# Kernel tuning notes

Hardware: AMD Instinct MI355X
Metric: run time of the kernel (lower is better)

## Reference

```python
import jax, jax.numpy as jnp
import numpy as np

IH, IW = 256, 704
FH, FW = 32, 88
D_MIN, D_MAX, D_RES = 1.0, 60.0, 0.5
D = int(np.ceil((D_MAX - D_MIN) / D_RES))  # 118 depth bins
C_IN, HID, C_OUT = 256, 64, 80
N_R, N_THETA = 128, 256
BN_EPS = 1e-5


def _edges():
    # non-uniform polar grid: angular bins uniform, radial bins grow with r
    ang = np.linspace(-np.pi / 2, np.pi / 2, N_THETA + 1).astype(np.float32)
    t = np.linspace(0.0, 1.0, N_R + 1)
    rad = (D_MIN + (t ** 1.5) * (D_MAX - D_MIN)).astype(np.float32)
    return jnp.asarray(ang), jnp.asarray(rad)


def _frustum():
    # [D, fH, fW, 3] of (u, v, depth) samples in image space
    ds = np.arange(D_MIN, D_MAX, D_RES, dtype=np.float32)
    xs = np.linspace(0, IW - 1, FW, dtype=np.float32)
    ys = np.linspace(0, IH - 1, FH, dtype=np.float32)
    d = np.broadcast_to(ds[:, None, None], (D, FH, FW))
    x = np.broadcast_to(xs[None, None, :], (D, FH, FW))
    y = np.broadcast_to(ys[None, :, None], (D, FH, FW))
    return jnp.asarray(np.stack([x, y, d], axis=-1))


def _bn(x, g, b, m, v):
    # inference-mode BatchNorm2d over channel axis 1; x: [BN, C, H, W]
    inv = g / jnp.sqrt(v + BN_EPS)
    return x * inv[None, :, None, None] + (b - m * inv)[None, :, None, None]


def setup_inputs() -> dict:
    key = jax.random.key(0)
    ks = jax.random.split(key, 8)
    B, N = 2, 1
    x = jax.random.normal(ks[0], (B, N, C_IN, FH, FW), dtype=jnp.float32)
    # camera->lidar axis permutation: x_l = z_c, y_l = -x_c, z_l = -y_c
    R = jnp.asarray([[0.0, 0.0, 1.0], [-1.0, 0.0, 0.0], [0.0, -1.0, 0.0]], dtype=jnp.float32)
    camera2lidar_rots = jnp.broadcast_to(R, (B, N, 3, 3))
    camera2lidar_trans = jnp.zeros((B, N, 3), dtype=jnp.float32)
    K = jnp.asarray([[380.0, 0.0, IW / 2.0], [0.0, 380.0, IH / 2.0], [0.0, 0.0, 1.0]], dtype=jnp.float32)
    intrins = jnp.broadcast_to(K, (B, N, 3, 3))
    s = 0.02
    params = dict(
        w1=jax.random.normal(ks[1], (HID, C_IN), dtype=jnp.float32) * s,
        b1=jnp.zeros((HID,), dtype=jnp.float32),
        g1=jnp.ones((HID,), dtype=jnp.float32),
        be1=jnp.zeros((HID,), dtype=jnp.float32),
        m1=jax.random.normal(ks[2], (HID,), dtype=jnp.float32) * s,
        v1=jnp.abs(jax.random.normal(ks[3], (HID,), dtype=jnp.float32)) + 0.5,
        w2=jax.random.normal(ks[4], (D + C_OUT, HID), dtype=jnp.float32) * s,
        b2=jnp.zeros((D + C_OUT,), dtype=jnp.float32),
        g2=jnp.ones((D + C_OUT,), dtype=jnp.float32),
        be2=jnp.zeros((D + C_OUT,), dtype=jnp.float32),
        m2=jax.random.normal(ks[5], (D + C_OUT,), dtype=jnp.float32) * s,
        v2=jnp.abs(jax.random.normal(ks[6], (D + C_OUT,), dtype=jnp.float32)) + 0.5,
    )
    return dict(x=x, camera2lidar_rots=camera2lidar_rots,
                camera2lidar_trans=camera2lidar_trans, intrins=intrins, **params)


def reference(x, camera2lidar_rots, camera2lidar_trans, intrins,
              w1, b1, g1, be1, m1, v1, w2, b2, g2, be2, m2, v2):
    B, N = x.shape[0], x.shape[1]
    # --- LIFT: DepthNet (two 1x1 convs + BN) -> depth dist x features outer product ---
    xf = x.reshape(B * N, C_IN, FH, FW)
    h = jnp.einsum('bchw,oc->bohw', xf, w1) + b1[None, :, None, None]
    h = jax.nn.relu(_bn(h, g1, be1, m1, v1))
    h = jnp.einsum('bchw,oc->bohw', h, w2) + b2[None, :, None, None]
    h = _bn(h, g2, be2, m2, v2)
    depth = jax.nn.softmax(h[:, :D], axis=1)            # [BN, D, fH, fW]
    feat = h[:, D:D + C_OUT]                            # [BN, C, fH, fW]
    lifted = depth[:, None, :, :, :] * feat[:, :, None, :, :]   # [BN, C, D, fH, fW]
    lifted = lifted.reshape(B, N, C_OUT, D, FH, FW).transpose(0, 1, 3, 4, 5, 2)  # [B,N,D,fH,fW,C]

    # --- geometry: unproject frustum to lidar frame ---
    fr = _frustum()                                      # [D, fH, fW, 3]
    u, v_, d = fr[..., 0], fr[..., 1], fr[..., 2]
    fx = intrins[..., 0, 0][:, :, None, None, None]
    fy = intrins[..., 1, 1][:, :, None, None, None]
    cx = intrins[..., 0, 2][:, :, None, None, None]
    cy = intrins[..., 1, 2][:, :, None, None, None]
    pc = jnp.stack([(u - cx) * d / fx, (v_ - cy) * d / fy,
                    jnp.broadcast_to(d, (B, N, D, FH, FW))], axis=-1)  # [B,N,D,fH,fW,3]
    pts = jnp.einsum('bnij,bndhwj->bndhwi', camera2lidar_rots, pc)
    pts = pts + camera2lidar_trans[:, :, None, None, None, :]

    # --- SPLAT: scatter-sum into non-uniform polar BEV grid ---
    ang_e, rad_e = _edges()
    xl, yl = pts[..., 0], pts[..., 1]
    r = jnp.sqrt(xl * xl + yl * yl)
    th = jnp.arctan2(yl, xl)
    r_idx = jnp.searchsorted(rad_e, r, side='right') - 1   # non-uniform bins -> bucketize
    t_idx = jnp.searchsorted(ang_e, th, side='right') - 1
    valid = (r_idx >= 0) & (r_idx < N_R) & (t_idx >= 0) & (t_idx < N_THETA)
    b_idx = jnp.arange(B)[:, None, None, None, None]
    trash = B * N_R * N_THETA  # dummy segment for out-of-grid points
    seg = jnp.where(valid, (b_idx * N_R + r_idx) * N_THETA + t_idx, trash).reshape(-1)
    bev = jax.ops.segment_sum(lifted.reshape(-1, C_OUT), seg, num_segments=trash + 1)[:-1]
    bev = bev.reshape(B, N_R, N_THETA, C_OUT).transpose(0, 3, 1, 2)  # [B, C, n_r, n_theta]
    return bev
```

## Files before the change

kernel.cpp:

```cpp
#include <hip/hip_runtime.h>
#include <hip/hip_bf16.h>
#include <math.h>

#define FH 32
#define FW 88
#define DD 118
#define C_IN 256
#define HID 64
#define C_OUT 80
#define NPIX 5632
#define PIX_PER_B 2816
#define N_R 128
#define N_THETA 256
#define NCOL 176
#define NBIN 32768
#define ECAP 12
#define PSTRIDE 9440

typedef __attribute__((ext_vector_type(8))) short short8;
typedef __attribute__((ext_vector_type(4))) float f32x4;

__device__ inline float bf2f(unsigned short h) {
  return __uint_as_float((unsigned)h << 16);
}
__device__ inline unsigned short f2bf(float f) {
  unsigned u = __float_as_uint(f);
  unsigned r = (u + 0x7fffu + ((u >> 16) & 1u)) >> 16;
  return (unsigned short)r;
}
__device__ inline bool detect_bf16(const void* intr) {
  float f = __uint_as_float(*(const unsigned*)intr);
  return !(f > 300.0f && f < 500.0f);
}
__device__ inline float ldf(const void* p, int i, bool isb) {
  return isb ? bf2f(((const unsigned short*)p)[i]) : ((const float*)p)[i];
}

__device__ inline void load_geom(int tid, float* radEL, float* angEL, float* camsL,
                                 const void* rots, const void* trans, const void* intr,
                                 bool isb) {
  if (tid < 129) {
    double t = (double)tid * (1.0 / 128.0);
    radEL[tid] = (float)(1.0 + pow(t, 1.5) * 59.0);
  }
  for (int i = tid; i < 257; i += 256) {
    double step = M_PI / 256.0;
    double vv = (i == 256) ? (M_PI / 2.0) : ((double)i * step + (-M_PI / 2.0));
    angEL[i] = (float)vv;
  }
  if (tid < 18) camsL[tid] = ldf(rots, tid, isb);
  if (tid < 6)  camsL[20 + tid] = ldf(trans, tid, isb);
  if (tid >= 6 && tid < 24) camsL[28 + (tid - 6)] = ldf(intr, tid - 6, isb);
}

__device__ inline int computeBin(int w, int h, int d,
                                 const float* camsF, int b,
                                 const float* radE, const float* angE) {
  float fx = camsF[28 + b * 9 + 0], cx = camsF[28 + b * 9 + 2];
  float fy = camsF[28 + b * 9 + 4], cy = camsF[28 + b * 9 + 5];
  float R00 = camsF[b * 9 + 0], R01 = camsF[b * 9 + 1], R02 = camsF[b * 9 + 2];
  float R10 = camsF[b * 9 + 3], R11 = camsF[b * 9 + 4], R12 = camsF[b * 9 + 5];
  float Tx = camsF[20 + b * 3 + 0], Ty = camsF[20 + b * 3 + 1];
  float u  = (w == FW - 1) ? 703.0f : (float)((double)w * (703.0 / 87.0));
  float vv = (h == FH - 1) ? 255.0f : (float)((double)h * (255.0 / 31.0));
  float dd = 1.0f + 0.5f * (float)d;
  float px = __fdiv_rn(__fmul_rn(__fsub_rn(u, cx), dd), fx);
  float py = __fdiv_rn(__fmul_rn(__fsub_rn(vv, cy), dd), fy);
  float xl = __fadd_rn(__fadd_rn(__fadd_rn(__fmul_rn(R00, px), __fmul_rn(R01, py)),
                                 __fmul_rn(R02, dd)), Tx);
  float yl = __fadd_rn(__fadd_rn(__fadd_rn(__fmul_rn(R10, px), __fmul_rn(R11, py)),
                                 __fmul_rn(R12, dd)), Ty);
  float r = __fsqrt_rn(__fadd_rn(__fmul_rn(xl, xl), __fmul_rn(yl, yl)));
  float th = (float)atan2((double)yl, (double)xl);
  int lo = 0, hi = 129;
  while (lo < hi) { int mid = (lo + hi) >> 1; if (radE[mid] <= r) lo = mid + 1; else hi = mid; }
  int ri = lo - 1;
  lo = 0; hi = 257;
  while (lo < hi) { int mid = (lo + hi) >> 1; if (angE[mid] <= th) lo = mid + 1; else hi = mid; }
  int ti = lo - 1;
  bool valid = (ri >= 0) && (ri < N_R) && (ti >= 0) && (ti < N_THETA);
  return valid ? (ri * N_THETA + ti) : -1;
}

__global__ __launch_bounds__(256) void k_bins(const void* __restrict__ rots,
                                              const void* __restrict__ trans,
                                              const void* __restrict__ intr,
                                              const void* __restrict__ b1r, const void* __restrict__ g1r,
                                              const void* __restrict__ be1r, const void* __restrict__ m1r,
                                              const void* __restrict__ v1r,
                                              const void* __restrict__ w2r, const void* __restrict__ b2r,
                                              const void* __restrict__ g2r, const void* __restrict__ be2r,
                                              const void* __restrict__ m2r, const void* __restrict__ v2r,
                                              int* __restrict__ cnt,
                                              unsigned* __restrict__ ent,
                                              int* __restrict__ flag,
                                              float* __restrict__ w2f, float* __restrict__ b2f,
                                              float* __restrict__ inv1G, float* __restrict__ b1fG) {
  int tid = threadIdx.x;
  bool isb = detect_bf16(intr);
  if (blockIdx.x >= 2640) {
    int j = (blockIdx.x - 2640) * 256 + tid;
    if (j < 12672) {
      int o = j >> 6;
      float iv = ldf(g2r, o, isb) / sqrtf(ldf(v2r, o, isb) + 1e-5f);
      w2f[j] = ldf(w2r, j, isb) * iv;
    } else if (j < 12870) {
      int o = j - 12672;
      float iv = ldf(g2r, o, isb) / sqrtf(ldf(v2r, o, isb) + 1e-5f);
      b2f[o] = ldf(b2r, o, isb) * iv + (ldf(be2r, o, isb) - ldf(m2r, o, isb) * iv);
    } else if (j < 12934) {
      int o = j - 12870;
      float iv = ldf(g1r, o, isb) / sqrtf(ldf(v1r, o, isb) + 1e-5f);
      inv1G[o] = iv;
      b1fG[o] = ldf(b1r, o, isb) * iv + (ldf(be1r, o, isb) - ldf(m1r, o, isb) * iv);
    }
    return;
  }
  __shared__ float radEL[129], angEL[257], camsL[46];
  __shared__ int bin0[8];
  __shared__ int varMask;
  int col = blockIdx.x / 15;
  int dchunk = blockIdx.x - col * 15;
  int b = col / FW, w = col - b * FW;
  int sub = tid >> 5, h = tid & 31;
  int d = dchunk * 8 + sub;
  if (tid == 0) varMask = 0;
  load_geom(tid, radEL, angEL, camsL, rots, trans, intr, isb);
  __syncthreads();
  int bin = -1;
  if (d < DD) bin = computeBin(w, h, d, camsL, b, radEL, angEL);
  if (d < DD && h == 0) bin0[sub] = bin;
  __syncthreads();
  if (d < DD && bin != bin0[sub]) atomicOr(&varMask, 1);
  __syncthreads();
  if (h == 0 && d < DD) {
    if (varMask) atomicOr(flag, 1);
    if (bin >= 0) {
      int slot = atomicAdd(&cnt[b * NBIN + bin], 1);
      if (slot < ECAP) ent[(size_t)(b * NBIN + bin) * ECAP + slot] = ((unsigned)col << 8) | (unsigned)d;
      else atomicOr(flag, 1);
    }
  }
}

__global__ __launch_bounds__(256) void k_mlp(const void* __restrict__ xraw,
                                             const void* __restrict__ intrRaw,
                                             const void* __restrict__ w1r,
                                             const float* __restrict__ w2f,
                                             const float* __restrict__ b2f,
                                             const float* __restrict__ inv1G,
                                             const float* __restrict__ b1fG,
                                             float* __restrict__ depthW,
                                             float* __restrict__ featW) {
  __shared__ __align__(16) float shbuf[3712];
  __shared__ __align__(16) float h1L[16 * 68];
  unsigned short* xsU = (unsigned short*)shbuf;
  float* h2s = shbuf;
  float* smaxL = shbuf + 3200;
  float* ssumL = shbuf + 3456;
  int tid = threadIdx.x;
  bool isb = detect_bf16(intrRaw);
  int pix0 = blockIdx.x * 16;
  int b = pix0 / PIX_PER_B;
  int ploc0 = pix0 - b * PIX_PER_B;
  size_t xbase = (size_t)b * C_IN * PIX_PER_B + ploc0;
  const unsigned short* xh = (const unsigned short*)xraw;
  const float* xf = (const float*)xraw;
  {
    int p = tid & 15, crow = tid >> 4;
    for (int it = 0; it < 16; it++) {
      int c = it * 16 + crow;
      size_t gi = xbase + (size_t)c * PIX_PER_B + p;
      xsU[p * 264 + c] = isb ? xh[gi] : f2bf(xf[gi]);
    }
  }
  int lane = tid & 63, wv = tid >> 6;
  int nloc = lane & 15, quad = lane >> 4;
  int orow = wv * 16 + nloc;
  short8 afr[8];
  const unsigned short* w1h = (const unsigned short*)w1r;
  const float* w1f32 = (const float*)w1r;
  if (isb) {
#pragma unroll
    for (int s = 0; s < 8; s++)
      afr[s] = *(const short8*)(w1h + orow * 256 + s * 32 + quad * 8);
  } else {
#pragma unroll
    for (int s = 0; s < 8; s++) {
      short8 a;
#pragma unroll
      for (int j = 0; j < 8; j++)
        a[j] = (short)f2bf(w1f32[orow * 256 + s * 32 + quad * 8 + j]);
      afr[s] = a;
    }
  }
  __syncthreads();
  f32x4 acc = {0.f, 0.f, 0.f, 0.f};
#pragma unroll
  for (int s = 0; s < 8; s++) {
    short8 bfr = *(const short8*)(xsU + nloc * 264 + s * 32 + quad * 8);
    acc = __builtin_amdgcn_mfma_f32_16x16x32_bf16(afr[s], bfr, acc, 0, 0, 0);
  }
#pragma unroll
  for (int r = 0; r < 4; r++) {
    int m = wv * 16 + quad * 4 + r;
    float hv = fmaxf(fmaf(acc[r], inv1G[m], b1fG[m]), 0.f);
    h1L[nloc * 68 + m] = hv;
  }
  __syncthreads();
  int p = tid & 15, g = tid >> 4;
  float h1v[64];
  const float4* hp = (const float4*)(h1L + p * 68);
#pragma unroll
  for (int k4 = 0; k4 < 16; k4++) {
    float4 hv = hp[k4];
    h1v[4 * k4 + 0] = hv.x; h1v[4 * k4 + 1] = hv.y;
    h1v[4 * k4 + 2] = hv.z; h1v[4 * k4 + 3] = hv.w;
  }
  for (int j = 0; j < 13; j++) {
    int o = g * 13 + j;
    if (o < 198) {
      float accs = b2f[o];
      const float4* wr = (const float4*)(w2f + o * 64);
#pragma unroll
      for (int k4 = 0; k4 < 16; k4++) {
        float4 w = wr[k4];
        accs = fmaf(w.x, h1v[4 * k4 + 0], accs);
        accs = fmaf(w.y, h1v[4 * k4 + 1], accs);
        accs = fmaf(w.z, h1v[4 * k4 + 2], accs);
        accs = fmaf(w.w, h1v[4 * k4 + 3], accs);
      }
      h2s[o * 16 + p] = accs;
    }
  }
  __syncthreads();
  int r0 = g * 8, r1 = min(118, r0 + 8);
  float lm = -INFINITY;
  for (int o = r0; o < r1; o++) lm = fmaxf(lm, h2s[o * 16 + p]);
  smaxL[g * 16 + p] = lm;
  __syncthreads();
  float m = smaxL[p];
#pragma unroll
  for (int gg = 1; gg < 16; gg++) m = fmaxf(m, smaxL[gg * 16 + p]);
  float ls = 0.f;
  for (int o = r0; o < r1; o++) ls += expf(h2s[o * 16 + p] - m);
  ssumL[g * 16 + p] = ls;
  __syncthreads();
  float tot = 0.f;
#pragma unroll
  for (int gg = 0; gg < 16; gg++) tot += ssumL[gg * 16 + p];
  int pix = pix0 + p;
  for (int o = r0; o < r1; o++)
    depthW[(size_t)pix * DD + o] = expf(h2s[o * 16 + p] - m) / tot;
  int f0 = g * 5;
  for (int f = f0; f < f0 + 5; f++)
    featW[(size_t)pix * C_OUT + f] = h2s[(118 + f) * 16 + p];
}

__global__ __launch_bounds__(256) void k_pcol(const float* __restrict__ depthW,
                                              const float* __restrict__ featW,
                                              const int* __restrict__ flag,
                                              float* __restrict__ P,
                                              float* __restrict__ bevAcc) {
  __shared__ float depthL[DD * 33];
  __shared__ __align__(16) float featL[FH * C_OUT];
  __shared__ int flagS;
  int tid = threadIdx.x;
  int col = blockIdx.x;
  int b = col / FW, w = col - b * FW;
  if (tid == 0) flagS = *flag;
  __syncthreads();
  if (flagS != 0) {
    float4 z = make_float4(0.f, 0.f, 0.f, 0.f);
    float4* bz = (float4*)bevAcc;
    for (int i = blockIdx.x * 256 + tid; i < (NBIN * 2 * C_OUT) / 4; i += 176 * 256) bz[i] = z;
    return;
  }
  size_t colPix = (size_t)b * PIX_PER_B + w;
  for (int i = tid; i < FH * DD; i += 256) {
    int h = i / DD, d = i - h * DD;
    depthL[d * 33 + h] = depthW[(colPix + (size_t)h * FW) * DD + d];
  }
  for (int i = tid; i < FH * C_OUT; i += 256) {
    int h = i / C_OUT, c = i - h * C_OUT;
    featL[i] = featW[(colPix + (size_t)h * FW) * C_OUT + c];
  }
  __syncthreads();
  const float4* featL4 = (const float4*)featL;
  float4* P4 = (float4*)(P + (size_t)col * PSTRIDE);
  for (int t = tid; t < DD * 20; t += 256) {
    int d = t / 20, c4 = t - d * 20;
    float4 a = make_float4(0.f, 0.f, 0.f, 0.f);
#pragma unroll
    for (int h = 0; h < FH; h++) {
      float wd = depthL[d * 33 + h];
      float4 f = featL4[h * 20 + c4];
      a.x = fmaf(wd, f.x, a.x); a.y = fmaf(wd, f.y, a.y);
      a.z = fmaf(wd, f.z, a.z); a.w = fmaf(wd, f.w, a.w);
    }
    P4[d * 20 + c4] = a;
  }
}

__global__ __launch_bounds__(256) void k_fb(const float* __restrict__ depthW,
                                            const float* __restrict__ featW,
                                            const int* __restrict__ flag,
                                            const void* __restrict__ rots,
                                            const void* __restrict__ trans,
                                            const void* __restrict__ intr,
                                            float* __restrict__ bevAcc) {
  if (*flag == 0) return;
  __shared__ float radEL[129], angEL[257], camsL[46];
  __shared__ float depthL[DD * 33];
  __shared__ __align__(16) float featL[FH * C_OUT];
  int tid = threadIdx.x;
  bool isb = detect_bf16(intr);
  int col = blockIdx.x >> 1, chalf = blockIdx.x & 1;
  int b = col / FW, w = col - b * FW;
  load_geom(tid, radEL, angEL, camsL, rots, trans, intr, isb);
  size_t colPix = (size_t)b * PIX_PER_B + w;
  for (int i = tid; i < FH * DD; i += 256) {
    int h = i / DD, d = i - h * DD;
    depthL[d * 33 + h] = depthW[(colPix + (size_t)h * FW) * DD + d];
  }
  for (int i = tid; i < FH * C_OUT; i += 256) {
    int h = i / C_OUT, c = i - h * C_OUT;
    featL[i] = featW[(colPix + (size_t)h * FW) * C_OUT + c];
  }
  __syncthreads();
  const float4* featL4 = (const float4*)featL;
  for (int t = tid; t < DD * FH * 10; t += 256) {
    int d = t / 320, rem = t - d * 320;
    int h = rem / 10, c4 = chalf * 10 + (rem - (rem / 10) * 10);
    int bin = computeBin(w, h, d, camsL, b, radEL, angEL);
    if (bin < 0) continue;
    float wd = depthL[d * 33 + h];
    float4 f = featL4[h * 20 + c4];
    float* outb = bevAcc + (((size_t)(b * C_OUT + c4 * 4)) << 15) + bin;
    unsafeAtomicAdd(outb, wd * f.x);
    unsafeAtomicAdd(outb + (1u << 15), wd * f.y);
    unsafeAtomicAdd(outb + (2u << 15), wd * f.z);
    unsafeAtomicAdd(outb + (3u << 15), wd * f.w);
  }
}

__global__ __launch_bounds__(256) void k_out(const float* __restrict__ P,
                                             const int* __restrict__ cnt,
                                             const unsigned* __restrict__ ent,
                                             const int* __restrict__ flag,
                                             const float* __restrict__ bevAcc,
                                             void* __restrict__ out,
                                             const void* __restrict__ intrRaw) {
  bool isb = detect_bf16(intrRaw);
  int tid = threadIdx.x;
  if (*flag != 0) {
    int idx = blockIdx.x * 256 + tid;
    const float4* a4 = (const float4*)bevAcc;
    int n4 = (NBIN * 2 * C_OUT) / 4;
    if (isb) {
      ushort4* o4 = (ushort4*)out;
      for (int i = idx; i < n4; i += 256 * 256) {
        float4 v = a4[i];
        ushort4 o; o.x = f2bf(v.x); o.y = f2bf(v.y); o.z = f2bf(v.z); o.w = f2bf(v.w);
        o4[i] = o;
      }
    } else {
      float4* o4 = (float4*)out;
      for (int i = idx; i < n4; i += 256 * 256) o4[i] = a4[i];
    }
    return;
  }
  int b = blockIdx.x >> 7, ri = blockIdx.x & 127;
  int ti = tid;
  int bin = ri * N_THETA + ti;
  int n = cnt[b * NBIN + bin];
  if (n > ECAP) n = ECAP;
  unsigned ee[ECAP];
  const unsigned* eb = ent + (size_t)(b * NBIN + bin) * ECAP;
  for (int i = 0; i < n; i++) ee[i] = eb[i];
  for (int i = 1; i < n; i++) {
    unsigned key = ee[i]; int j = i - 1;
    while (j >= 0 && ee[j] > key) { ee[j + 1] = ee[j]; j--; }
    ee[j + 1] = key;
  }
  int base[ECAP];
  for (int i = 0; i < n; i++)
    base[i] = (int)(((ee[i] >> 8) * PSTRIDE + (ee[i] & 255u) * C_OUT) >> 2);
  const float4* P4 = (const float4*)P;
  unsigned short* oh = (unsigned short*)out;
  float* of = (float*)out;
  size_t obase = (((size_t)(b * C_OUT)) << 15) + bin;
  for (int c4 = 0; c4 < 20; c4++) {
    float4 s = make_float4(0.f, 0.f, 0.f, 0.f);
    for (int i = 0; i < n; i++) {
      float4 v = P4[base[i] + c4];
      s.x += v.x; s.y += v.y; s.z += v.z; s.w += v.w;
    }
    size_t o0 = obase + ((size_t)(c4 * 4) << 15);
    if (isb) {
      oh[o0]              = f2bf(s.x);
      oh[o0 + (1u << 15)] = f2bf(s.y);
      oh[o0 + (2u << 15)] = f2bf(s.z);
      oh[o0 + (3u << 15)] = f2bf(s.w);
    } else {
      of[o0]              = s.x;
      of[o0 + (1u << 15)] = s.y;
      of[o0 + (2u << 15)] = s.z;
      of[o0 + (3u << 15)] = s.w;
    }
  }
}

extern "C" void kernel_launch(void* const* d_in, const int* in_sizes, int n_in,
                              void* d_out, int out_size, void* d_ws, size_t ws_size,
                              hipStream_t stream) {
  const void* x     = d_in[0];
  const void* rots  = d_in[1];
  const void* trans = d_in[2];
  const void* intr  = d_in[3];
  const void* w1  = d_in[4];
  const void* b1  = d_in[5];
  const void* g1  = d_in[6];
  const void* be1 = d_in[7];
  const void* m1  = d_in[8];
  const void* v1  = d_in[9];
  const void* w2  = d_in[10];
  const void* b2  = d_in[11];
  const void* g2  = d_in[12];
  const void* be2 = d_in[13];
  const void* m2  = d_in[14];
  const void* v2  = d_in[15];

  float* ws = (float*)d_ws;
  float*    bevAcc = ws + 0;
  float*    P      = ws + 0;
  int*      cnt    = (int*)(ws + 1661440);
  int*      flag   = (int*)(ws + 1726976);
  unsigned* ent    = (unsigned*)(ws + 1727040);
  float*    depthW = ws + 5242880;
  float*    featW  = ws + 5907456;
  float*    w2f    = ws + 6358016;
  float*    b2f    = ws + 6370688;
  float*    inv1G  = ws + 6370912;
  float*    b1fG   = ws + 6370976;

  (void)hipMemsetAsync(cnt, 0, (size_t)(65536 + 64) * sizeof(int), stream);
  k_bins<<<2691, 256, 0, stream>>>(rots, trans, intr,
                                   b1, g1, be1, m1, v1,
                                   w2, b2, g2, be2, m2, v2,
                                   cnt, ent, flag, w2f, b2f, inv1G, b1fG);
  k_mlp<<<NPIX / 16, 256, 0, stream>>>(x, intr, w1, w2f, b2f, inv1G, b1fG, depthW, featW);
  k_pcol<<<NCOL, 256, 0, stream>>>(depthW, featW, flag, P, bevAcc);
  k_fb<<<NCOL * 2, 256, 0, stream>>>(depthW, featW, flag, rots, trans, intr, bevAcc);
  k_out<<<256, 256, 0, stream>>>(P, cnt, ent, flag, bevAcc, d_out, intr);
}
```

Measured before the change: 156.2 us.

## Fuse bins and MLP into one front kernel and merge pcol/fallback kernels

Merges the bin-computation, BN-folding and MLP kernels into one launch partitioned by block index. BN folding is now done per MLP block in shared memory and applied on the fly to the raw w2 weights, instead of being precomputed into global buffers. The fallback accumulator zeroing moves into the front kernel, and the P-column and fallback kernels are merged into one launch. This cuts launch count and inter-kernel serialization, at the cost of redundant BN math per block and unconditional zeroing of bevAcc, which now sits in its own workspace region.

```diff
diff --git a/kernel.cpp b/kernel.cpp
--- a/kernel.cpp
+++ b/kernel.cpp
@@ -16,6 +16,11 @@
 #define NBIN 32768
 #define ECAP 12
 #define PSTRIDE 9440
+
+#define FRONT_MLP  352
+#define FRONT_BINS 2640
+#define FRONT_ZERO 320
+#define FRONT_TOTAL (FRONT_MLP + FRONT_BINS + FRONT_ZERO)
 
 typedef __attribute__((ext_vector_type(8))) short short8;
 typedef __attribute__((ext_vector_type(4))) float f32x4;
@@ -82,84 +87,79 @@
   return valid ? (ri * N_THETA + ti) : -1;
 }
 
-__global__ __launch_bounds__(256) void k_bins(const void* __restrict__ rots,
-                                              const void* __restrict__ trans,
-                                              const void* __restrict__ intr,
-                                              const void* __restrict__ b1r, const void* __restrict__ g1r,
-                                              const void* __restrict__ be1r, const void* __restrict__ m1r,
-                                              const void* __restrict__ v1r,
-                                              const void* __restrict__ w2r, const void* __restrict__ b2r,
-                                              const void* __restrict__ g2r, const void* __restrict__ be2r,
-                                              const void* __restrict__ m2r, const void* __restrict__ v2r,
-                                              int* __restrict__ cnt,
-                                              unsigned* __restrict__ ent,
-                                              int* __restrict__ flag,
-                                              float* __restrict__ w2f, float* __restrict__ b2f,
-                                              float* __restrict__ inv1G, float* __restrict__ b1fG) {
-  int tid = threadIdx.x;
-  bool isb = detect_bf16(intr);
-  if (blockIdx.x >= 2640) {
-    int j = (blockIdx.x - 2640) * 256 + tid;
-    if (j < 12672) {
-      int o = j >> 6;
-      float iv = ldf(g2r, o, isb) / sqrtf(ldf(v2r, o, isb) + 1e-5f);
-      w2f[j] = ldf(w2r, j, isb) * iv;
-    } else if (j < 12870) {
-      int o = j - 12672;
-      float iv = ldf(g2r, o, isb) / sqrtf(ldf(v2r, o, isb) + 1e-5f);
-      b2f[o] = ldf(b2r, o, isb) * iv + (ldf(be2r, o, isb) - ldf(m2r, o, isb) * iv);
-    } else if (j < 12934) {
-      int o = j - 12870;
-      float iv = ldf(g1r, o, isb) / sqrtf(ldf(v1r, o, isb) + 1e-5f);
-      inv1G[o] = iv;
-      b1fG[o] = ldf(b1r, o, isb) * iv + (ldf(be1r, o, isb) - ldf(m1r, o, isb) * iv);
-    }
-    return;
-  }
+__global__ __launch_bounds__(256) void k_front(
+    const void* __restrict__ xraw,
+    const void* __restrict__ rots, const void* __restrict__ trans,
+    const void* __restrict__ intr,
+    const void* __restrict__ w1r, const void* __restrict__ b1r,
+    const void* __restrict__ g1r, const void* __restrict__ be1r,
+    const void* __restrict__ m1r, const void* __restrict__ v1r,
+    const void* __restrict__ w2r, const void* __restrict__ b2r,
+    const void* __restrict__ g2r, const void* __restrict__ be2r,
+    const void* __restrict__ m2r, const void* __restrict__ v2r,
+    int* __restrict__ cnt, unsigned* __restrict__ ent, int* __restrict__ flag,
+    float* __restrict__ depthW, float* __restrict__ featW,
+    float* __restrict__ bevAcc) {
+  __shared__ __align__(16) float shbuf[3712];
+  __shared__ __align__(16) float h1L[16 * 68];
+  __shared__ float inv1L[64], b1fL[64], inv2L[198], b2fL[198];
   __shared__ float radEL[129], angEL[257], camsL[46];
   __shared__ int bin0[8];
   __shared__ int varMask;
-  int col = blockIdx.x / 15;
-  int dchunk = blockIdx.x - col * 15;
-  int b = col / FW, w = col - b * FW;
-  int sub = tid >> 5, h = tid & 31;
-  int d = dchunk * 8 + sub;
-  if (tid == 0) varMask = 0;
-  load_geom(tid, radEL, angEL, camsL, rots, trans, intr, isb);
-  __syncthreads();
-  int bin = -1;
-  if (d < DD) bin = computeBin(w, h, d, camsL, b, radEL, angEL);
-  if (d < DD && h == 0) bin0[sub] = bin;
-  __syncthreads();
-  if (d < DD && bin != bin0[sub]) atomicOr(&varMask, 1);
-  __syncthreads();
-  if (h == 0 && d < DD) {
-    if (varMask) atomicOr(flag, 1);
-    if (bin >= 0) {
-      int slot = atomicAdd(&cnt[b * NBIN + bin], 1);
-      if (slot < ECAP) ent[(size_t)(b * NBIN + bin) * ECAP + slot] = ((unsigned)col << 8) | (unsigned)d;
-      else atomicOr(flag, 1);
-    }
-  }
-}
-
-__global__ __launch_bounds__(256) void k_mlp(const void* __restrict__ xraw,
-                                             const void* __restrict__ intrRaw,
-                                             const void* __restrict__ w1r,
-                                             const float* __restrict__ w2f,
-                                             const float* __restrict__ b2f,
-                                             const float* __restrict__ inv1G,
-                                             const float* __restrict__ b1fG,
-                                             float* __restrict__ depthW,
-                                             float* __restrict__ featW) {
-  __shared__ __align__(16) float shbuf[3712];
-  __shared__ __align__(16) float h1L[16 * 68];
+
+  int tid = threadIdx.x;
+  bool isb = detect_bf16(intr);
+
+  if (blockIdx.x >= FRONT_MLP + FRONT_BINS) {
+    int zb = blockIdx.x - (FRONT_MLP + FRONT_BINS);
+    float4 z = make_float4(0.f, 0.f, 0.f, 0.f);
+    float4* bz = (float4*)bevAcc;
+    int n4 = (NBIN * 2 * C_OUT) / 4;
+    for (int i = zb * 256 + tid; i < n4; i += FRONT_ZERO * 256) bz[i] = z;
+    return;
+  }
+
+  if (blockIdx.x >= FRONT_MLP) {
+    int bb = blockIdx.x - FRONT_MLP;
+    int col = bb / 15;
+    int dchunk = bb - col * 15;
+    int b = col / FW, w = col - b * FW;
+    int sub = tid >> 5, h = tid & 31;
+    int d = dchunk * 8 + sub;
+    if (tid == 0) varMask = 0;
+    load_geom(tid, radEL, angEL, camsL, rots, trans, intr, isb);
+    __syncthreads();
+    int bin = -1;
+    if (d < DD) bin = computeBin(w, h, d, camsL, b, radEL, angEL);
+    if (d < DD && h == 0) bin0[sub] = bin;
+    __syncthreads();
+    if (d < DD && bin != bin0[sub]) atomicOr(&varMask, 1);
+    __syncthreads();
+    if (h == 0 && d < DD) {
+      if (varMask) atomicOr(flag, 1);
+      if (bin >= 0) {
+        int slot = atomicAdd(&cnt[b * NBIN + bin], 1);
+        if (slot < ECAP) ent[(size_t)(b * NBIN + bin) * ECAP + slot] = ((unsigned)col << 8) | (unsigned)d;
+        else atomicOr(flag, 1);
+      }
+    }
+    return;
+  }
+
   unsigned short* xsU = (unsigned short*)shbuf;
   float* h2s = shbuf;
   float* smaxL = shbuf + 3200;
   float* ssumL = shbuf + 3456;
-  int tid = threadIdx.x;
-  bool isb = detect_bf16(intrRaw);
+  if (tid < 64) {
+    float iv = ldf(g1r, tid, isb) / sqrtf(ldf(v1r, tid, isb) + 1e-5f);
+    inv1L[tid] = iv;
+    b1fL[tid] = ldf(b1r, tid, isb) * iv + (ldf(be1r, tid, isb) - ldf(m1r, tid, isb) * iv);
+  }
+  if (tid < 198) {
+    float iv = ldf(g2r, tid, isb) / sqrtf(ldf(v2r, tid, isb) + 1e-5f);
+    inv2L[tid] = iv;
+    b2fL[tid] = ldf(b2r, tid, isb) * iv + (ldf(be2r, tid, isb) - ldf(m2r, tid, isb) * iv);
+  }
   int pix0 = blockIdx.x * 16;
   int b = pix0 / PIX_PER_B;
   int ploc0 = pix0 - b * PIX_PER_B;
@@ -204,7 +204,7 @@
 #pragma unroll
   for (int r = 0; r < 4; r++) {
     int m = wv * 16 + quad * 4 + r;
-    float hv = fmaxf(fmaf(acc[r], inv1G[m], b1fG[m]), 0.f);
+    float hv = fmaxf(fmaf(acc[r], inv1L[m], b1fL[m]), 0.f);
     h1L[nloc * 68 + m] = hv;
   }
   __syncthreads();
@@ -220,15 +220,28 @@
   for (int j = 0; j < 13; j++) {
     int o = g * 13 + j;
     if (o < 198) {
-      float accs = b2f[o];
-      const float4* wr = (const float4*)(w2f + o * 64);
-#pragma unroll
-      for (int k4 = 0; k4 < 16; k4++) {
-        float4 w = wr[k4];
-        accs = fmaf(w.x, h1v[4 * k4 + 0], accs);
-        accs = fmaf(w.y, h1v[4 * k4 + 1], accs);
-        accs = fmaf(w.z, h1v[4 * k4 + 2], accs);
-        accs = fmaf(w.w, h1v[4 * k4 + 3], accs);
+      float iv = inv2L[o];
+      float accs = b2fL[o];
+      if (isb) {
+        const ushort4* wr = (const ushort4*)w2r;
+#pragma unroll
+        for (int k4 = 0; k4 < 16; k4++) {
+          ushort4 uw = wr[o * 16 + k4];
+          accs = fmaf(bf2f(uw.x) * iv, h1v[4 * k4 + 0], accs);
+          accs = fmaf(bf2f(uw.y) * iv, h1v[4 * k4 + 1], accs);
+          accs = fmaf(bf2f(uw.z) * iv, h1v[4 * k4 + 2], accs);
+          accs = fmaf(bf2f(uw.w) * iv, h1v[4 * k4 + 3], accs);
+        }
+      } else {
+        const float4* wr = (const float4*)w2r;
+#pragma unroll
+        for (int k4 = 0; k4 < 16; k4++) {
+          float4 w = wr[o * 16 + k4];
+          accs = fmaf(w.x * iv, h1v[4 * k4 + 0], accs);
+          accs = fmaf(w.y * iv, h1v[4 * k4 + 1], accs);
+          accs = fmaf(w.z * iv, h1v[4 * k4 + 2], accs);
+          accs = fmaf(w.w * iv, h1v[4 * k4 + 3], accs);
+        }
       }
       h2s[o * 16 + p] = accs;
     }
@@ -257,65 +270,57 @@
     featW[(size_t)pix * C_OUT + f] = h2s[(118 + f) * 16 + p];
 }
 
-__global__ __launch_bounds__(256) void k_pcol(const float* __restrict__ depthW,
+__global__ __launch_bounds__(256) void k_back(const float* __restrict__ depthW,
                                               const float* __restrict__ featW,
                                               const int* __restrict__ flag,
+                                              const void* __restrict__ rots,
+                                              const void* __restrict__ trans,
+                                              const void* __restrict__ intr,
                                               float* __restrict__ P,
                                               float* __restrict__ bevAcc) {
   __shared__ float depthL[DD * 33];
   __shared__ __align__(16) float featL[FH * C_OUT];
+  __shared__ float radEL[129], angEL[257], camsL[46];
   __shared__ int flagS;
   int tid = threadIdx.x;
-  int col = blockIdx.x;
-  int b = col / FW, w = col - b * FW;
   if (tid == 0) flagS = *flag;
   __syncthreads();
-  if (flagS != 0) {
-    float4 z = make_float4(0.f, 0.f, 0.f, 0.f);
-    float4* bz = (float4*)bevAcc;
-    for (int i = blockIdx.x * 256 + tid; i < (NBIN * 2 * C_OUT) / 4; i += 176 * 256) bz[i] = z;
+
+  if (blockIdx.x < NCOL) {
+    if (flagS != 0) return;
+    int col = blockIdx.x;
+    int b = col / FW, w = col - b * FW;
+    size_t colPix = (size_t)b * PIX_PER_B + w;
+    for (int i = tid; i < FH * DD; i += 256) {
+      int h = i / DD, d = i - h * DD;
+      depthL[d * 33 + h] = depthW[(colPix + (size_t)h * FW) * DD + d];
+    }
+    for (int i = tid; i < FH * C_OUT; i += 256) {
+      int h = i / C_OUT, c = i - h * C_OUT;
+      featL[i] = featW[(colPix + (size_t)h * FW) * C_OUT + c];
+    }
+    __syncthreads();
+    const float4* featL4 = (const float4*)featL;
+    float4* P4 = (float4*)(P + (size_t)col * PSTRIDE);
+    for (int t = tid; t < DD * 20; t += 256) {
+      int d = t / 20, c4 = t - d * 20;
+      float4 a = make_float4(0.f, 0.f, 0.f, 0.f);
+#pragma unroll
+      for (int h = 0; h < FH; h++) {
+        float wd = depthL[d * 33 + h];
+        float4 f = featL4[h * 20 + c4];
+        a.x = fmaf(wd, f.x, a.x); a.y = fmaf(wd, f.y, a.y);
+        a.z = fmaf(wd, f.z, a.z); a.w = fmaf(wd, f.w, a.w);
+      }
+      P4[d * 20 + c4] = a;
+    }
     return;
   }
-  size_t colPix = (size_t)b * PIX_PER_B + w;
-  for (int i = tid; i < FH * DD; i += 256) {
-    int h = i / DD, d = i - h * DD;
-    depthL[d * 33 + h] = depthW[(colPix + (size_t)h * FW) * DD + d];
-  }
-  for (int i = tid; i < FH * C_OUT; i += 256) {
-    int h = i / C_OUT, c = i - h * C_OUT;
-    featL[i] = featW[(colPix + (size_t)h * FW) * C_OUT + c];
-  }
-  __syncthreads();
-  const float4* featL4 = (const float4*)featL;
-  float4* P4 = (float4*)(P + (size_t)col * PSTRIDE);
-  for (int t = tid; t < DD * 20; t += 256) {
-    int d = t / 20, c4 = t - d * 20;
-    float4 a = make_float4(0.f, 0.f, 0.f, 0.f);
-#pragma unroll
-    for (int h = 0; h < FH; h++) {
-      float wd = depthL[d * 33 + h];
-      float4 f = featL4[h * 20 + c4];
-      a.x = fmaf(wd, f.x, a.x); a.y = fmaf(wd, f.y, a.y);
-      a.z = fmaf(wd, f.z, a.z); a.w = fmaf(wd, f.w, a.w);
-    }
-    P4[d * 20 + c4] = a;
-  }
-}
-
-__global__ __launch_bounds__(256) void k_fb(const float* __restrict__ depthW,
-                                            const float* __restrict__ featW,
-                                            const int* __restrict__ flag,
-                                            const void* __restrict__ rots,
-                                            const void* __restrict__ trans,
-                                            const void* __restrict__ intr,
-                                            float* __restrict__ bevAcc) {
-  if (*flag == 0) return;
-  __shared__ float radEL[129], angEL[257], camsL[46];
-  __shared__ float depthL[DD * 33];
-  __shared__ __align__(16) float featL[FH * C_OUT];
-  int tid = threadIdx.x;
+
+  if (flagS == 0) return;
   bool isb = detect_bf16(intr);
-  int col = blockIdx.x >> 1, chalf = blockIdx.x & 1;
+  int idx2 = blockIdx.x - NCOL;
+  int col = idx2 >> 1, chalf = idx2 & 1;
   int b = col / FW, w = col - b * FW;
   load_geom(tid, radEL, angEL, camsL, rots, trans, intr, isb);
   size_t colPix = (size_t)b * PIX_PER_B + w;
@@ -432,25 +437,19 @@
   const void* v2  = d_in[15];
 
   float* ws = (float*)d_ws;
-  float*    bevAcc = ws + 0;
   float*    P      = ws + 0;
   int*      cnt    = (int*)(ws + 1661440);
   int*      flag   = (int*)(ws + 1726976);
   unsigned* ent    = (unsigned*)(ws + 1727040);
-  float*    depthW = ws + 5242880;
-  float*    featW  = ws + 5907456;
-  float*    w2f    = ws + 6358016;
-  float*    b2f    = ws + 6370688;
-  float*    inv1G  = ws + 6370912;
-  float*    b1fG   = ws + 6370976;
+  float*    depthW = ws + 2513472;
+  float*    featW  = ws + 3178048;
+  float*    bevAcc = ws + 3628608;
 
   (void)hipMemsetAsync(cnt, 0, (size_t)(65536 + 64) * sizeof(int), stream);
-  k_bins<<<2691, 256, 0, stream>>>(rots, trans, intr,
-                                   b1, g1, be1, m1, v1,
-                                   w2, b2, g2, be2, m2, v2,
-                                   cnt, ent, flag, w2f, b2f, inv1G, b1fG);
-  k_mlp<<<NPIX / 16, 256, 0, stream>>>(x, intr, w1, w2f, b2f, inv1G, b1fG, depthW, featW);
-  k_pcol<<<NCOL, 256, 0, stream>>>(depthW, featW, flag, P, bevAcc);
-  k_fb<<<NCOL * 2, 256, 0, stream>>>(depthW, featW, flag, rots, trans, intr, bevAcc);
+  k_front<<<FRONT_TOTAL, 256, 0, stream>>>(x, rots, trans, intr,
+                                           w1, b1, g1, be1, m1, v1,
+                                           w2, b2, g2, be2, m2, v2,
+                                           cnt, ent, flag, depthW, featW, bevAcc);
+  k_back<<<NCOL * 3, 256, 0, stream>>>(depthW, featW, flag, rots, trans, intr, P, bevAcc);
   k_out<<<256, 256, 0, stream>>>(P, cnt, ent, flag, bevAcc, d_out, intr);
 }
```

After: 149.2 us. 1.05x faster.
